# Performance work log

Hardware: AMD Instinct MI355X
Metric: run time of the kernel (lower is better)

## Reference

```python
import jax, jax.numpy as jnp
import numpy as np

# Eigenvalue spec: (alpha, omega, multiplicity); field='complex' => d_state = sum(mul)
EIGS = [(-0.4, 0.0, 32), (-0.3, 3.14, 32), (-0.2, 6.28, 32), (-0.1, 12.57, 32),
        (-0.05, 25.13, 32), (-0.02, 50.27, 32), (-0.01, 100.53, 32), (-0.005, 201.06, 32)]
DELTA_MIN, DELTA_MAX = 1e-3, 1e-1
B_SZ, H, L = 8, 128, 8192  # batch, d_input, seq length


def setup_inputs() -> dict:
    key = jax.random.key(0)
    k_delta, k_bre, k_bim, k_cre, k_cim, k_d, k_u = jax.random.split(key, 7)
    # continuous-time diagonal state matrix Lambda (P,) complex
    Lam = np.concatenate([np.full(m, a + 1j * w, dtype=np.complex64) for a, w, m in EIGS])
    Lambda = jnp.asarray(Lam)  # (P,)
    P = Lambda.shape[0]
    # ZOH discretization (done at init in the torch module)
    Delta = DELTA_MIN + (DELTA_MAX - DELTA_MIN) * jax.random.uniform(k_delta, (P,), dtype=jnp.float32)
    Lambda_bar = jnp.exp(Lambda * Delta)  # (P,) complex64
    B = (jax.random.normal(k_bre, (P, H), dtype=jnp.float32)
         + 1j * jax.random.normal(k_bim, (P, H), dtype=jnp.float32))
    B_bar = (((Lambda_bar - 1.0) / Lambda)[:, None] * B).astype(jnp.complex64)  # (P,H)
    C_re = jax.random.normal(k_cre, (H, P), dtype=jnp.float32)
    C_im = jax.random.normal(k_cim, (H, P), dtype=jnp.float32)
    D = jax.random.normal(k_d, (H, H), dtype=jnp.float32)
    u = jax.random.normal(k_u, (B_SZ, H, L), dtype=jnp.float32)
    return {
        "u": u,
        "Lambda_bar_re": jnp.real(Lambda_bar), "Lambda_bar_im": jnp.imag(Lambda_bar),
        "B_bar_re": jnp.real(B_bar), "B_bar_im": jnp.imag(B_bar),
        "C_re": C_re, "C_im": C_im, "D": D,
    }


def reference(u, Lambda_bar_re, Lambda_bar_im, B_bar_re, B_bar_im, C_re, C_im, D):
    Lambda_bar = Lambda_bar_re + 1j * Lambda_bar_im          # (P,)
    B_bar = B_bar_re + 1j * B_bar_im                         # (P,H)
    C = C_re + 1j * C_im                                     # (H,P)
    uc = u.astype(B_bar.dtype)
    Bu = jnp.einsum('ph,bhl->bpl', B_bar, uc)                # (B,P,L) complex
    A = jnp.broadcast_to(Lambda_bar[None, :, None], Bu.shape)  # (B,P,L)
    # The repo's binary op computes the sequential recurrence x_t = A_t * (x_{t-1} + Bu_t).
    # Rewriting with Bu'_t = A_t * Bu_t gives x_t = A_t x_{t-1} + Bu'_t, which is the
    # standard (truly associative) first-order scan.
    ABu = A * Bu

    def binop(ei, ej):
        a_i, b_i = ei
        a_j, b_j = ej
        return a_j * a_i, a_j * b_i + b_j

    _, xs = jax.lax.associative_scan(binop, (A, ABu), axis=2)  # xs: (B,P,L)
    y = jnp.einsum('op,bpl->bol', C, xs).real + jnp.einsum('oh,bhl->bol', D, u)
    return jax.nn.gelu(y, approximate=False)  # torch nn.GELU default = exact erf
```

## Files before the change

kernel.cpp:

```cpp
#include <hip/hip_runtime.h>
#include <math.h>

#define Bn 8
#define Hd 128
#define Ld 8192
#define Pd 256
#define LC 32
#define NC 256

typedef __attribute__((ext_vector_type(8))) short bf16x8;
typedef __attribute__((ext_vector_type(4))) float f32x4;
#define MFMA16(a, b, c) __builtin_amdgcn_mfma_f32_16x16x32_bf16(a, b, c, 0, 0, 0)

__device__ __forceinline__ unsigned short f2bf(float f) {
  unsigned u = __float_as_uint(f);
  u = u + 0x7fffu + ((u >> 16) & 1u);
  return (unsigned short)(u >> 16);
}

#if __has_builtin(__builtin_amdgcn_cvt_pk_bf16_f32)
typedef __attribute__((ext_vector_type(2))) __bf16 v2bf_t;
__device__ __forceinline__ unsigned pack2(float a, float b) {
  v2bf_t r = __builtin_amdgcn_cvt_pk_bf16_f32(a, b);
  unsigned u;
  __builtin_memcpy(&u, &r, 4);
  return u;
}
#else
__device__ __forceinline__ unsigned pack2(float a, float b) {
  return (unsigned)f2bf(a) | ((unsigned)f2bf(b) << 16);
}
#endif

__device__ __forceinline__ float bflo(unsigned v) { return __uint_as_float(v << 16); }
__device__ __forceinline__ float bfhi(unsigned v) { return __uint_as_float(v & 0xffff0000u); }

__device__ __forceinline__ int bperm(int p) {
  return ((p & 4) << 2) | ((p & 16) >> 1) | ((p & 8) >> 1) | (p & 3);
}

__global__ void k_prep(const float* __restrict__ Bre, const float* __restrict__ Bim,
                       const float* __restrict__ Cre, const float* __restrict__ Cim,
                       const float* __restrict__ Dm,
                       bf16x8* __restrict__ Bfr, bf16x8* __restrict__ Bfi,
                       bf16x8* __restrict__ Cf, bf16x8* __restrict__ Df) {
  int tid = blockIdx.x * 256 + threadIdx.x;
  int lane = tid & 63, slot = tid >> 6;
  int q = lane >> 4, ln = lane & 15;
  if (slot < 64) {
    int ks = slot >> 4, mt = slot & 15;
    int p = mt * 16 + ln;
    bf16x8 vr, vi;
#pragma unroll
    for (int e = 0; e < 8; ++e) {
      int h = ks * 32 + q * 8 + e;
      vr[e] = (short)f2bf(Bre[p * Hd + h]);
      vi[e] = (short)f2bf(Bim[p * Hd + h]);
    }
    Bfr[slot * 64 + lane] = vr;
    Bfi[slot * 64 + lane] = vi;
  } else if (slot < 64 + 128) {
    int s2 = slot - 64;
    int ks = s2 >> 3, mt = s2 & 7;
    int o = mt * 16 + ln;
    bf16x8 v;
#pragma unroll
    for (int e = 0; e < 8; ++e) {
      int kp = ks * 32 + q * 8 + e;
      int p = kp >> 1;
      float val = (kp & 1) ? -Cim[o * Pd + p] : Cre[o * Pd + p];
      v[e] = (short)f2bf(val);
    }
    Cf[s2 * 64 + lane] = v;
  } else if (slot < 64 + 128 + 32) {
    int s3 = slot - 192;
    int ks = s3 >> 3, mt = s3 & 7;
    int o = mt * 16 + ln;
    bf16x8 v;
#pragma unroll
    for (int e = 0; e < 8; ++e) {
      int h = ks * 32 + q * 8 + e;
      v[e] = (short)f2bf(Dm[o * Hd + h]);
    }
    Df[s3 * 64 + lane] = v;
  }
}

__device__ __forceinline__ void stage_u(const float* __restrict__ ub, unsigned* us32, int t) {
  int lane = t & 63, w = t >> 6;
  int j0 = 4 * (lane & 7);
  int h2 = 16 * w + 2 * (lane >> 3);
  const float* r0 = ub + (size_t)h2 * Ld + j0;
  float4 a0 = *(const float4*)r0;
  float4 a1 = *(const float4*)(r0 + Ld);
  const float* r2 = r0 + (size_t)64 * Ld;
  float4 b0 = *(const float4*)r2;
  float4 b1 = *(const float4*)(r2 + Ld);
  float ta0[4] = {a0.x, a0.y, a0.z, a0.w};
  float ta1[4] = {a1.x, a1.y, a1.z, a1.w};
  float tb0[4] = {b0.x, b0.y, b0.z, b0.w};
  float tb1[4] = {b1.x, b1.y, b1.z, b1.w};
#pragma unroll
  for (int i = 0; i < 4; ++i) {
    int j = j0 + i;
    int g1 = (h2 >> 3) ^ (j & 7);
    us32[(j * 256 + (g1 << 4) + ((2 * h2) & 15)) >> 2] = pack2(ta0[i], ta1[i]);
    int hb = h2 + 64;
    int g2 = (hb >> 3) ^ (j & 7);
    us32[(j * 256 + (g2 << 4) + ((2 * hb) & 15)) >> 2] = pack2(tb0[i], tb1[i]);
  }
}

__device__ __forceinline__ void compute_bu(const unsigned* us32,
                                           const bf16x8* __restrict__ Bfr,
                                           const bf16x8* __restrict__ Bfi,
                                           unsigned* bu32, int t) {
  int lane = t & 63, w = t >> 6, q = lane >> 4, ln = lane & 15;
  f32x4 zz = {0.f, 0.f, 0.f, 0.f};
  f32x4 aR[4][2], aI[4][2];
#pragma unroll
  for (int mt = 0; mt < 4; ++mt)
#pragma unroll
    for (int n = 0; n < 2; ++n) { aR[mt][n] = zz; aI[mt][n] = zz; }

#pragma unroll
  for (int ks = 0; ks < 4; ++ks) {
    bf16x8 ubf[2];
#pragma unroll
    for (int n = 0; n < 2; ++n) {
      int j = 16 * n + ln;
      int g = (4 * ks + q) ^ (j & 7);
      ubf[n] = *(const bf16x8*)((const char*)us32 + j * 256 + g * 16);
    }
#pragma unroll
    for (int mt = 0; mt < 4; ++mt) {
      int tI = ks * 16 + w * 4 + mt;
      bf16x8 ar = Bfr[tI * 64 + lane];
      bf16x8 ai = Bfi[tI * 64 + lane];
#pragma unroll
      for (int n = 0; n < 2; ++n) {
        aR[mt][n] = MFMA16(ar, ubf[n], aR[mt][n]);
        aI[mt][n] = MFMA16(ai, ubf[n], aI[mt][n]);
      }
    }
  }
#pragma unroll
  for (int mt = 0; mt < 4; ++mt)
#pragma unroll
    for (int n = 0; n < 2; ++n)
#pragma unroll
      for (int r = 0; r < 4; ++r) {
        int p = w * 64 + mt * 16 + q * 4 + r;
        int j = 16 * n + ln;
        bu32[(p << 5) | (j ^ bperm(p))] = pack2(aR[mt][n][r], aI[mt][n][r]);
      }
}

__global__ __launch_bounds__(256, 4) void k_chunk(
    const float* __restrict__ u, const float* __restrict__ lre,
    const float* __restrict__ lim, const bf16x8* __restrict__ Bfr,
    const bf16x8* __restrict__ Bfi, float2* __restrict__ E) {
  int bc = blockIdx.x;
  int b = bc >> 8, c = bc & 255;
  __shared__ __align__(16) unsigned char smem[8192 + 32768];
  unsigned* us32 = (unsigned*)smem;
  unsigned* bu32 = (unsigned*)(smem + 8192);
  int t = threadIdx.x;

  stage_u(u + (size_t)b * Hd * Ld + c * LC, us32, t);
  __syncthreads();
  compute_bu(us32, Bfr, Bfi, bu32, t);
  __syncthreads();

  int p = t;
  int pm = bperm(p);
  float ax = lre[p], ay = lim[p];
  float xr = 0.f, xi = 0.f;
#pragma unroll
  for (int j = 0; j < LC; ++j) {
    unsigned v = bu32[(p << 5) | (j ^ pm)];
    float sr = xr + bflo(v), si = xi + bfhi(v);
    xr = ax * sr - ay * si;
    xi = ax * si + ay * sr;
  }
  E[(size_t)bc * Pd + p] = make_float2(xr, xi);
}

__global__ __launch_bounds__(256) void k_scan(const float* __restrict__ lre,
                                              const float* __restrict__ lim,
                                              float2* __restrict__ E) {
  __shared__ float2 arr[32][8];
  int nb = blockIdx.x;
  int t = threadIdx.x;
  int pl = t & 7, rq = t >> 3;
  int b = nb >> 5;
  int p = ((nb & 31) << 3) + pl;
  float ax = lre[p], ay = lim[p];
  float mx = ax, my = ay;
#pragma unroll
  for (int k = 0; k < 5; ++k) {
    float nx = mx * mx - my * my, ny = 2.f * mx * my;
    mx = nx; my = ny;
  }
  size_t base = ((size_t)(b * NC + rq * 8)) * Pd + p;
  float2 pre[8];
  float cr = 0.f, ci = 0.f;
#pragma unroll
  for (int i = 0; i < 8; ++i) {
    float2 e = E[base + (size_t)i * Pd];
    pre[i] = make_float2(cr, ci);
    float nx = mx * cr - my * ci + e.x;
    float ny = mx * ci + my * cr + e.y;
    cr = nx; ci = ny;
  }
  float Mx = mx, My = my;
#pragma unroll
  for (int k = 0; k < 3; ++k) {
    float nx = Mx * Mx - My * My, ny = 2.f * Mx * My;
    Mx = nx; My = ny;
  }
  float Vx = cr, Vy = ci;
#pragma unroll
  for (int d = 1; d < 32; d <<= 1) {
    arr[rq][pl] = make_float2(Vx, Vy);
    __syncthreads();
    if (rq >= d) {
      float2 pv = arr[rq - d][pl];
      Vx += Mx * pv.x - My * pv.y;
      Vy += Mx * pv.y + My * pv.x;
    }
    __syncthreads();
    float nx = Mx * Mx - My * My, ny = 2.f * Mx * My;
    Mx = nx; My = ny;
  }
  arr[rq][pl] = make_float2(Vx, Vy);
  __syncthreads();
  float Cx = 0.f, Cy = 0.f;
  if (rq > 0) {
    float2 pv = arr[rq - 1][pl];
    Cx = pv.x; Cy = pv.y;
  }
  float tx = 1.f, ty = 0.f;
#pragma unroll
  for (int i = 0; i < 8; ++i) {
    float ox = pre[i].x + tx * Cx - ty * Cy;
    float oy = pre[i].y + tx * Cy + ty * Cx;
    E[base + (size_t)i * Pd] = make_float2(ox, oy);
    float nx = tx * mx - ty * my, ny = tx * my + ty * mx;
    tx = nx; ty = ny;
  }
}

__global__ __launch_bounds__(256, 4) void k_main(
    const float* __restrict__ u, const float* __restrict__ lre,
    const float* __restrict__ lim, const bf16x8* __restrict__ Bfr,
    const bf16x8* __restrict__ Bfi, const bf16x8* __restrict__ Cf,
    const bf16x8* __restrict__ Df, const float2* __restrict__ E,
    float* __restrict__ out) {
  int bc = blockIdx.x;
  int b = bc >> 8, c = bc & 255;
  __shared__ __align__(16) unsigned char smem[8192 + 32768];
  unsigned* us32 = (unsigned*)smem;
  unsigned* bu32 = (unsigned*)(smem + 8192);
  unsigned* xs32 = bu32;
  int t = threadIdx.x;
  int lane = t & 63, w = t >> 6, q = lane >> 4, ln = lane & 15;

  stage_u(u + (size_t)b * Hd * Ld + c * LC, us32, t);
  __syncthreads();
  compute_bu(us32, Bfr, Bfi, bu32, t);
  __syncthreads();

  int p = t;
  int pm = bperm(p);
  unsigned v[LC];
#pragma unroll
  for (int j = 0; j < LC; ++j) v[j] = bu32[(p << 5) | (j ^ pm)];
  float2 xin = E[(size_t)bc * Pd + p];
  __syncthreads();

  {
    float ax = lre[p], ay = lim[p];
    float xr = xin.x, xi = xin.y;
#pragma unroll
    for (int j = 0; j < LC; ++j) {
      float sr = xr + bflo(v[j]), si = xi + bfhi(v[j]);
      xr = ax * sr - ay * si;
      xi = ax * si + ay * sr;
      xs32[j * 256 + ((((p >> 2) ^ (j & 7)) << 2) + (p & 3))] = pack2(xr, xi);
    }
  }
  __syncthreads();

  f32x4 zz = {0.f, 0.f, 0.f, 0.f};
  f32x4 acc[2][2] = {{zz, zz}, {zz, zz}};
#pragma unroll
  for (int ks = 0; ks < 16; ++ks) {
    bf16x8 xb[2];
#pragma unroll
    for (int n = 0; n < 2; ++n) {
      int j = 16 * n + ln;
      int g = (4 * ks + q) ^ (j & 7);
      xb[n] = *(const bf16x8*)((const char*)xs32 + j * 1024 + g * 16);
    }
#pragma unroll
    for (int mt = 0; mt < 2; ++mt) {
      bf16x8 cf = Cf[(ks * 8 + w * 2 + mt) * 64 + lane];
#pragma unroll
      for (int n = 0; n < 2; ++n) acc[mt][n] = MFMA16(cf, xb[n], acc[mt][n]);
    }
  }
#pragma unroll
  for (int ks = 0; ks < 4; ++ks) {
    bf16x8 ubf[2];
#pragma unroll
    for (int n = 0; n < 2; ++n) {
      int j = 16 * n + ln;
      int g = (4 * ks + q) ^ (j & 7);
      ubf[n] = *(const bf16x8*)((const char*)us32 + j * 256 + g * 16);
    }
#pragma unroll
    for (int mt = 0; mt < 2; ++mt) {
      bf16x8 df = Df[(ks * 8 + w * 2 + mt) * 64 + lane];
#pragma unroll
      for (int n = 0; n < 2; ++n) acc[mt][n] = MFMA16(df, ubf[n], acc[mt][n]);
    }
  }

#pragma unroll
  for (int mt = 0; mt < 2; ++mt)
#pragma unroll
    for (int n = 0; n < 2; ++n)
#pragma unroll
      for (int r = 0; r < 4; ++r) {
        int o = w * 32 + mt * 16 + q * 4 + r;
        int l = c * LC + 16 * n + ln;
        float vy = acc[mt][n][r];
        float e2 = __builtin_amdgcn_exp2f(-2.4554670f * vy);
        float gy = vy * __builtin_amdgcn_rcpf(1.0f + e2);
        out[((size_t)(b * Hd + o)) * Ld + l] = gy;
      }
}

extern "C" void kernel_launch(void* const* d_in, const int* in_sizes, int n_in,
                              void* d_out, int out_size, void* d_ws, size_t ws_size,
                              hipStream_t stream) {
  const float* u   = (const float*)d_in[0];
  const float* lre = (const float*)d_in[1];
  const float* lim = (const float*)d_in[2];
  const float* Bre = (const float*)d_in[3];
  const float* Bim = (const float*)d_in[4];
  const float* Cre = (const float*)d_in[5];
  const float* Cim = (const float*)d_in[6];
  const float* Dm  = (const float*)d_in[7];
  float* out = (float*)d_out;

  char* ws = (char*)d_ws;
  bf16x8* Bfr = (bf16x8*)(ws);
  bf16x8* Bfi = (bf16x8*)(ws + 65536);
  bf16x8* Cf  = (bf16x8*)(ws + 131072);
  bf16x8* Df  = (bf16x8*)(ws + 262144);
  float2* E   = (float2*)(ws + (1 << 20));

  k_prep<<<56, 256, 0, stream>>>(Bre, Bim, Cre, Cim, Dm, Bfr, Bfi, Cf, Df);
  k_chunk<<<Bn * NC, 256, 0, stream>>>(u, lre, lim, Bfr, Bfi, E);
  k_scan<<<256, 256, 0, stream>>>(lre, lim, E);
  k_main<<<Bn * NC, 256, 0, stream>>>(u, lre, lim, Bfr, Bfi, Cf, Df, E, out);
}
```

Measured before the change: 147.5 us.

## Fuse chunk, scan and projection into one cooperative persistent kernel

Replaces the three-kernel chunk/scan/main sequence with one cooperative kernel of 1024 blocks that each handle two chunks. Grid-wide syncs separate the chunk-state, cross-chunk scan and projection phases. The Bu values are kept in registers between phases so the B projection and recurrence inputs are not recomputed in the final phase, and launch gaps are removed. The cost is two grid barriers, higher register pressure from holding 64 packed values per thread, and only 256 of 1024 blocks working during the scan phase; the old three-kernel path remains as a fallback if the cooperative launch is not available.

```diff
diff --git a/kernel.cpp b/kernel.cpp
--- a/kernel.cpp
+++ b/kernel.cpp
@@ -1,5 +1,8 @@
 #include <hip/hip_runtime.h>
+#include <hip/hip_cooperative_groups.h>
 #include <math.h>
+
+namespace cg = cooperative_groups;
 
 #define Bn 8
 #define Hd 128
@@ -156,6 +159,247 @@
       }
 }
 
+__device__ __forceinline__ void compute_bu_half(const unsigned* us32,
+                                                const bf16x8* __restrict__ Bfr,
+                                                const bf16x8* __restrict__ Bfi,
+                                                unsigned* bu32, int t, int mh) {
+  int lane = t & 63, w = t >> 6, q = lane >> 4, ln = lane & 15;
+  f32x4 zz = {0.f, 0.f, 0.f, 0.f};
+  f32x4 aR[2][2], aI[2][2];
+#pragma unroll
+  for (int mt = 0; mt < 2; ++mt)
+#pragma unroll
+    for (int n = 0; n < 2; ++n) { aR[mt][n] = zz; aI[mt][n] = zz; }
+
+#pragma unroll
+  for (int ks = 0; ks < 4; ++ks) {
+    bf16x8 ubf[2];
+#pragma unroll
+    for (int n = 0; n < 2; ++n) {
+      int j = 16 * n + ln;
+      int g = (4 * ks + q) ^ (j & 7);
+      ubf[n] = *(const bf16x8*)((const char*)us32 + j * 256 + g * 16);
+    }
+#pragma unroll
+    for (int mt = 0; mt < 2; ++mt) {
+      int tI = ks * 16 + w * 4 + mh * 2 + mt;
+      bf16x8 ar = Bfr[tI * 64 + lane];
+      bf16x8 ai = Bfi[tI * 64 + lane];
+#pragma unroll
+      for (int n = 0; n < 2; ++n) {
+        aR[mt][n] = MFMA16(ar, ubf[n], aR[mt][n]);
+        aI[mt][n] = MFMA16(ai, ubf[n], aI[mt][n]);
+      }
+    }
+  }
+#pragma unroll
+  for (int mt = 0; mt < 2; ++mt)
+#pragma unroll
+    for (int n = 0; n < 2; ++n)
+#pragma unroll
+      for (int r = 0; r < 4; ++r) {
+        int p = w * 64 + (mh * 2 + mt) * 16 + q * 4 + r;
+        int j = 16 * n + ln;
+        bu32[(p << 5) | (j ^ bperm(p))] = pack2(aR[mt][n][r], aI[mt][n][r]);
+      }
+}
+
+__device__ __forceinline__ void scan_rows(const float* __restrict__ lre,
+                                          const float* __restrict__ lim,
+                                          float2* __restrict__ E, int nb, int t,
+                                          float2* arr) {
+  int pl = t & 7, rq = t >> 3;
+  int b = nb >> 5;
+  int p = ((nb & 31) << 3) + pl;
+  float mx = lre[p], my = lim[p];
+#pragma unroll
+  for (int k = 0; k < 5; ++k) {
+    float nx = mx * mx - my * my, ny = 2.f * mx * my;
+    mx = nx; my = ny;
+  }
+  size_t base = ((size_t)(b * NC + rq * 8)) * Pd + p;
+  float2 pre[8];
+  float cr = 0.f, ci = 0.f;
+#pragma unroll
+  for (int i = 0; i < 8; ++i) {
+    float2 e = E[base + (size_t)i * Pd];
+    pre[i] = make_float2(cr, ci);
+    float nx = mx * cr - my * ci + e.x;
+    float ny = mx * ci + my * cr + e.y;
+    cr = nx; ci = ny;
+  }
+  float Mx = mx, My = my;
+#pragma unroll
+  for (int k = 0; k < 3; ++k) {
+    float nx = Mx * Mx - My * My, ny = 2.f * Mx * My;
+    Mx = nx; My = ny;
+  }
+  float Vx = cr, Vy = ci;
+#pragma unroll
+  for (int d = 1; d < 32; d <<= 1) {
+    arr[rq * 8 + pl] = make_float2(Vx, Vy);
+    __syncthreads();
+    if (rq >= d) {
+      float2 pv = arr[(rq - d) * 8 + pl];
+      Vx += Mx * pv.x - My * pv.y;
+      Vy += Mx * pv.y + My * pv.x;
+    }
+    __syncthreads();
+    float nx = Mx * Mx - My * My, ny = 2.f * Mx * My;
+    Mx = nx; My = ny;
+  }
+  arr[rq * 8 + pl] = make_float2(Vx, Vy);
+  __syncthreads();
+  float Cx = 0.f, Cy = 0.f;
+  if (rq > 0) {
+    float2 pv = arr[(rq - 1) * 8 + pl];
+    Cx = pv.x; Cy = pv.y;
+  }
+  float tx = 1.f, ty = 0.f;
+#pragma unroll
+  for (int i = 0; i < 8; ++i) {
+    float ox = pre[i].x + tx * Cx - ty * Cy;
+    float oy = pre[i].y + tx * Cy + ty * Cx;
+    E[base + (size_t)i * Pd] = make_float2(ox, oy);
+    float nx = tx * mx - ty * my, ny = tx * my + ty * mx;
+    tx = nx; ty = ny;
+  }
+}
+
+__device__ __forceinline__ void project_one(const bf16x8* __restrict__ Cf,
+                                            const bf16x8* __restrict__ Df,
+                                            const unsigned* us32, const unsigned* xs32,
+                                            float* __restrict__ out, int b, int c, int t) {
+  int lane = t & 63, w = t >> 6, q = lane >> 4, ln = lane & 15;
+  f32x4 zz = {0.f, 0.f, 0.f, 0.f};
+  f32x4 acc[2][2] = {{zz, zz}, {zz, zz}};
+#pragma unroll
+  for (int ks = 0; ks < 16; ++ks) {
+    bf16x8 xb[2];
+#pragma unroll
+    for (int n = 0; n < 2; ++n) {
+      int j = 16 * n + ln;
+      int g = (4 * ks + q) ^ (j & 7);
+      xb[n] = *(const bf16x8*)((const char*)xs32 + j * 1024 + g * 16);
+    }
+#pragma unroll
+    for (int mt = 0; mt < 2; ++mt) {
+      bf16x8 cf = Cf[(ks * 8 + w * 2 + mt) * 64 + lane];
+#pragma unroll
+      for (int n = 0; n < 2; ++n) acc[mt][n] = MFMA16(cf, xb[n], acc[mt][n]);
+    }
+  }
+#pragma unroll
+  for (int ks = 0; ks < 4; ++ks) {
+    bf16x8 ubf[2];
+#pragma unroll
+    for (int n = 0; n < 2; ++n) {
+      int j = 16 * n + ln;
+      int g = (4 * ks + q) ^ (j & 7);
+      ubf[n] = *(const bf16x8*)((const char*)us32 + j * 256 + g * 16);
+    }
+#pragma unroll
+    for (int mt = 0; mt < 2; ++mt) {
+      bf16x8 df = Df[(ks * 8 + w * 2 + mt) * 64 + lane];
+#pragma unroll
+      for (int n = 0; n < 2; ++n) acc[mt][n] = MFMA16(df, ubf[n], acc[mt][n]);
+    }
+  }
+#pragma unroll
+  for (int mt = 0; mt < 2; ++mt)
+#pragma unroll
+    for (int n = 0; n < 2; ++n)
+#pragma unroll
+      for (int r = 0; r < 4; ++r) {
+        int o = w * 32 + mt * 16 + q * 4 + r;
+        int l = c * LC + 16 * n + ln;
+        float vy = acc[mt][n][r];
+        float e2 = __builtin_amdgcn_exp2f(-2.4554670f * vy);
+        float gy = vy * __builtin_amdgcn_rcpf(1.0f + e2);
+        out[((size_t)(b * Hd + o)) * Ld + l] = gy;
+      }
+}
+
+__device__ __forceinline__ void phaseA_one(const float* __restrict__ u,
+                                           const bf16x8* __restrict__ Bfr,
+                                           const bf16x8* __restrict__ Bfi,
+                                           float2* __restrict__ E, unsigned* us32,
+                                           unsigned* bu32, int t, int bc, float ax,
+                                           float ay, int pm, unsigned (&vv)[LC]) {
+  int b = bc >> 8, c = bc & 255;
+  int p = t;
+  stage_u(u + (size_t)b * Hd * Ld + c * LC, us32, t);
+  __syncthreads();
+  compute_bu_half(us32, Bfr, Bfi, bu32, t, 0);
+  compute_bu_half(us32, Bfr, Bfi, bu32, t, 1);
+  __syncthreads();
+  float xr = 0.f, xi = 0.f;
+#pragma unroll
+  for (int j = 0; j < LC; ++j) {
+    unsigned w = bu32[(p << 5) | (j ^ pm)];
+    vv[j] = w;
+    float sr = xr + bflo(w), si = xi + bfhi(w);
+    xr = ax * sr - ay * si;
+    xi = ax * si + ay * sr;
+  }
+  E[(size_t)bc * Pd + p] = make_float2(xr, xi);
+}
+
+template <bool RESTAGE>
+__device__ __forceinline__ void phaseC_one(const float* __restrict__ u,
+                                           const bf16x8* __restrict__ Cf,
+                                           const bf16x8* __restrict__ Df,
+                                           const float2* __restrict__ E,
+                                           float* __restrict__ out, unsigned* us32,
+                                           unsigned* xs32, int t, int bc, float ax,
+                                           float ay, const unsigned (&vv)[LC]) {
+  int b = bc >> 8, c = bc & 255;
+  int p = t;
+  if (RESTAGE) stage_u(u + (size_t)b * Hd * Ld + c * LC, us32, t);
+  float2 xin = E[(size_t)bc * Pd + p];
+  float xr = xin.x, xi = xin.y;
+#pragma unroll
+  for (int j = 0; j < LC; ++j) {
+    unsigned w = vv[j];
+    float sr = xr + bflo(w), si = xi + bfhi(w);
+    xr = ax * sr - ay * si;
+    xi = ax * si + ay * sr;
+    xs32[j * 256 + ((((p >> 2) ^ (j & 7)) << 2) + (p & 3))] = pack2(xr, xi);
+  }
+  __syncthreads();
+  project_one(Cf, Df, us32, xs32, out, b, c, t);
+}
+
+__global__ __launch_bounds__(256, 4) void k_fused(
+    const float* __restrict__ u, const float* __restrict__ lre,
+    const float* __restrict__ lim, const bf16x8* __restrict__ Bfr,
+    const bf16x8* __restrict__ Bfi, const bf16x8* __restrict__ Cf,
+    const bf16x8* __restrict__ Df, float2* __restrict__ E,
+    float* __restrict__ out) {
+  cg::grid_group grid = cg::this_grid();
+  int blk = blockIdx.x;
+  __shared__ __align__(16) unsigned char smem[8192 + 32768];
+  unsigned* us32 = (unsigned*)smem;
+  unsigned* bu32 = (unsigned*)(smem + 8192);
+  int t = threadIdx.x;
+  int p = t, pm = bperm(p);
+  float ax = lre[p], ay = lim[p];
+  unsigned v0[LC], v1[LC];
+
+  phaseA_one(u, Bfr, Bfi, E, us32, bu32, t, 2 * blk + 0, ax, ay, pm, v0);
+  phaseA_one(u, Bfr, Bfi, E, us32, bu32, t, 2 * blk + 1, ax, ay, pm, v1);
+  __threadfence();
+  grid.sync();
+
+  if (blk < 256) scan_rows(lre, lim, E, blk, t, (float2*)bu32);
+  __threadfence();
+  grid.sync();
+
+  phaseC_one<false>(u, Cf, Df, E, out, us32, bu32, t, 2 * blk + 1, ax, ay, v1);
+  __syncthreads();
+  phaseC_one<true>(u, Cf, Df, E, out, us32, bu32, t, 2 * blk + 0, ax, ay, v0);
+}
+
 __global__ __launch_bounds__(256, 4) void k_chunk(
     const float* __restrict__ u, const float* __restrict__ lre,
     const float* __restrict__ lim, const bf16x8* __restrict__ Bfr,
@@ -189,66 +433,8 @@
 __global__ __launch_bounds__(256) void k_scan(const float* __restrict__ lre,
                                               const float* __restrict__ lim,
                                               float2* __restrict__ E) {
-  __shared__ float2 arr[32][8];
-  int nb = blockIdx.x;
-  int t = threadIdx.x;
-  int pl = t & 7, rq = t >> 3;
-  int b = nb >> 5;
-  int p = ((nb & 31) << 3) + pl;
-  float ax = lre[p], ay = lim[p];
-  float mx = ax, my = ay;
-#pragma unroll
-  for (int k = 0; k < 5; ++k) {
-    float nx = mx * mx - my * my, ny = 2.f * mx * my;
-    mx = nx; my = ny;
-  }
-  size_t base = ((size_t)(b * NC + rq * 8)) * Pd + p;
-  float2 pre[8];
-  float cr = 0.f, ci = 0.f;
-#pragma unroll
-  for (int i = 0; i < 8; ++i) {
-    float2 e = E[base + (size_t)i * Pd];
-    pre[i] = make_float2(cr, ci);
-    float nx = mx * cr - my * ci + e.x;
-    float ny = mx * ci + my * cr + e.y;
-    cr = nx; ci = ny;
-  }
-  float Mx = mx, My = my;
-#pragma unroll
-  for (int k = 0; k < 3; ++k) {
-    float nx = Mx * Mx - My * My, ny = 2.f * Mx * My;
-    Mx = nx; My = ny;
-  }
-  float Vx = cr, Vy = ci;
-#pragma unroll
-  for (int d = 1; d < 32; d <<= 1) {
-    arr[rq][pl] = make_float2(Vx, Vy);
-    __syncthreads();
-    if (rq >= d) {
-      float2 pv = arr[rq - d][pl];
-      Vx += Mx * pv.x - My * pv.y;
-      Vy += Mx * pv.y + My * pv.x;
-    }
-    __syncthreads();
-    float nx = Mx * Mx - My * My, ny = 2.f * Mx * My;
-    Mx = nx; My = ny;
-  }
-  arr[rq][pl] = make_float2(Vx, Vy);
-  __syncthreads();
-  float Cx = 0.f, Cy = 0.f;
-  if (rq > 0) {
-    float2 pv = arr[rq - 1][pl];
-    Cx = pv.x; Cy = pv.y;
-  }
-  float tx = 1.f, ty = 0.f;
-#pragma unroll
-  for (int i = 0; i < 8; ++i) {
-    float ox = pre[i].x + tx * Cx - ty * Cy;
-    float oy = pre[i].y + tx * Cy + ty * Cx;
-    E[base + (size_t)i * Pd] = make_float2(ox, oy);
-    float nx = tx * mx - ty * my, ny = tx * my + ty * mx;
-    tx = nx; ty = ny;
-  }
+  __shared__ float2 arr[32 * 8];
+  scan_rows(lre, lim, E, blockIdx.x, threadIdx.x, arr);
 }
 
 __global__ __launch_bounds__(256, 4) void k_main(
@@ -264,7 +450,6 @@
   unsigned* bu32 = (unsigned*)(smem + 8192);
   unsigned* xs32 = bu32;
   int t = threadIdx.x;
-  int lane = t & 63, w = t >> 6, q = lane >> 4, ln = lane & 15;
 
   stage_u(u + (size_t)b * Hd * Ld + c * LC, us32, t);
   __syncthreads();
@@ -291,55 +476,7 @@
     }
   }
   __syncthreads();
-
-  f32x4 zz = {0.f, 0.f, 0.f, 0.f};
-  f32x4 acc[2][2] = {{zz, zz}, {zz, zz}};
-#pragma unroll
-  for (int ks = 0; ks < 16; ++ks) {
-    bf16x8 xb[2];
-#pragma unroll
-    for (int n = 0; n < 2; ++n) {
-      int j = 16 * n + ln;
-      int g = (4 * ks + q) ^ (j & 7);
-      xb[n] = *(const bf16x8*)((const char*)xs32 + j * 1024 + g * 16);
-    }
-#pragma unroll
-    for (int mt = 0; mt < 2; ++mt) {
-      bf16x8 cf = Cf[(ks * 8 + w * 2 + mt) * 64 + lane];
-#pragma unroll
-      for (int n = 0; n < 2; ++n) acc[mt][n] = MFMA16(cf, xb[n], acc[mt][n]);
-    }
-  }
-#pragma unroll
-  for (int ks = 0; ks < 4; ++ks) {
-    bf16x8 ubf[2];
-#pragma unroll
-    for (int n = 0; n < 2; ++n) {
-      int j = 16 * n + ln;
-      int g = (4 * ks + q) ^ (j & 7);
-      ubf[n] = *(const bf16x8*)((const char*)us32 + j * 256 + g * 16);
-    }
-#pragma unroll
-    for (int mt = 0; mt < 2; ++mt) {
-      bf16x8 df = Df[(ks * 8 + w * 2 + mt) * 64 + lane];
-#pragma unroll
-      for (int n = 0; n < 2; ++n) acc[mt][n] = MFMA16(df, ubf[n], acc[mt][n]);
-    }
-  }
-
-#pragma unroll
-  for (int mt = 0; mt < 2; ++mt)
-#pragma unroll
-    for (int n = 0; n < 2; ++n)
-#pragma unroll
-      for (int r = 0; r < 4; ++r) {
-        int o = w * 32 + mt * 16 + q * 4 + r;
-        int l = c * LC + 16 * n + ln;
-        float vy = acc[mt][n][r];
-        float e2 = __builtin_amdgcn_exp2f(-2.4554670f * vy);
-        float gy = vy * __builtin_amdgcn_rcpf(1.0f + e2);
-        out[((size_t)(b * Hd + o)) * Ld + l] = gy;
-      }
+  project_one(Cf, Df, us32, xs32, out, b, c, t);
 }
 
 extern "C" void kernel_launch(void* const* d_in, const int* in_sizes, int n_in,
@@ -362,7 +499,25 @@
   bf16x8* Df  = (bf16x8*)(ws + 262144);
   float2* E   = (float2*)(ws + (1 << 20));
 
+  static int coop = -1;
+  if (coop < 0) {
+    int nb = 0;
+    hipError_t oe = hipOccupancyMaxActiveBlocksPerMultiprocessor(&nb, k_fused, 256, 0);
+    coop = (oe == hipSuccess && nb >= 4) ? 1 : 0;
+  }
+
   k_prep<<<56, 256, 0, stream>>>(Bre, Bim, Cre, Cim, Dm, Bfr, Bfi, Cf, Df);
+
+  if (coop == 1) {
+    void* kargs[] = {(void*)&u,   (void*)&lre, (void*)&lim, (void*)&Bfr,
+                     (void*)&Bfi, (void*)&Cf,  (void*)&Df,  (void*)&E,
+                     (void*)&out};
+    hipError_t err = hipLaunchCooperativeKernel((void*)k_fused, dim3(1024),
+                                                dim3(256), kargs, 0, stream);
+    if (err == hipSuccess) return;
+    coop = 0;
+  }
+
   k_chunk<<<Bn * NC, 256, 0, stream>>>(u, lre, lim, Bfr, Bfi, E);
   k_scan<<<256, 256, 0, stream>>>(lre, lim, E);
   k_main<<<Bn * NC, 256, 0, stream>>>(u, lre, lim, Bfr, Bfi, Cf, Df, E, out);
```

Result: no change. 148.4 us (+0.6%).

## Compute zero-state chunk output in first pass, add carried-state correction later

Applied to the files above, without the earlier changes.

The first chunk kernel now computes the zero-initial-state scan output C·x0 + D·u and writes it to a workspace buffer. The final kernel then only adds the contribution of the incoming carry, which is a geometric series in Lambda_bar times the carry, so it no longer restages u or recomputes B·u. This removes the duplicate Bu GEMM and u load from the second pass. In exchange it adds a full-size fp32 intermediate write and read, of the same size as the output, plus extra MFMA work in the first pass.

```diff
diff --git a/kernel.cpp b/kernel.cpp
--- a/kernel.cpp
+++ b/kernel.cpp
@@ -156,16 +156,20 @@
       }
 }
 
-__global__ __launch_bounds__(256, 4) void k_chunk(
+__global__ __launch_bounds__(256, 4) void k_chunkP(
     const float* __restrict__ u, const float* __restrict__ lre,
     const float* __restrict__ lim, const bf16x8* __restrict__ Bfr,
-    const bf16x8* __restrict__ Bfi, float2* __restrict__ E) {
+    const bf16x8* __restrict__ Bfi, const bf16x8* __restrict__ Cf,
+    const bf16x8* __restrict__ Df, float2* __restrict__ E,
+    float* __restrict__ p0out) {
   int bc = blockIdx.x;
   int b = bc >> 8, c = bc & 255;
   __shared__ __align__(16) unsigned char smem[8192 + 32768];
   unsigned* us32 = (unsigned*)smem;
   unsigned* bu32 = (unsigned*)(smem + 8192);
+  unsigned* xs32 = bu32;
   int t = threadIdx.x;
+  int lane = t & 63, w = t >> 6, q = lane >> 4, ln = lane & 15;
 
   stage_u(u + (size_t)b * Hd * Ld + c * LC, us32, t);
   __syncthreads();
@@ -174,16 +178,68 @@
 
   int p = t;
   int pm = bperm(p);
-  float ax = lre[p], ay = lim[p];
-  float xr = 0.f, xi = 0.f;
-#pragma unroll
-  for (int j = 0; j < LC; ++j) {
-    unsigned v = bu32[(p << 5) | (j ^ pm)];
-    float sr = xr + bflo(v), si = xi + bfhi(v);
-    xr = ax * sr - ay * si;
-    xi = ax * si + ay * sr;
-  }
-  E[(size_t)bc * Pd + p] = make_float2(xr, xi);
+  unsigned v[LC];
+#pragma unroll
+  for (int j = 0; j < LC; ++j) v[j] = bu32[(p << 5) | (j ^ pm)];
+  __syncthreads();
+
+  {
+    float ax = lre[p], ay = lim[p];
+    float xr = 0.f, xi = 0.f;
+#pragma unroll
+    for (int j = 0; j < LC; ++j) {
+      float sr = xr + bflo(v[j]), si = xi + bfhi(v[j]);
+      xr = ax * sr - ay * si;
+      xi = ax * si + ay * sr;
+      xs32[j * 256 + ((((p >> 2) ^ (j & 7)) << 2) + (p & 3))] = pack2(xr, xi);
+    }
+    E[(size_t)bc * Pd + p] = make_float2(xr, xi);
+  }
+  __syncthreads();
+
+  f32x4 zz = {0.f, 0.f, 0.f, 0.f};
+  f32x4 acc[2][2] = {{zz, zz}, {zz, zz}};
+#pragma unroll
+  for (int ks = 0; ks < 16; ++ks) {
+    bf16x8 xb[2];
+#pragma unroll
+    for (int n = 0; n < 2; ++n) {
+      int j = 16 * n + ln;
+      int g = (4 * ks + q) ^ (j & 7);
+      xb[n] = *(const bf16x8*)((const char*)xs32 + j * 1024 + g * 16);
+    }
+#pragma unroll
+    for (int mt = 0; mt < 2; ++mt) {
+      bf16x8 cf = Cf[(ks * 8 + w * 2 + mt) * 64 + lane];
+#pragma unroll
+      for (int n = 0; n < 2; ++n) acc[mt][n] = MFMA16(cf, xb[n], acc[mt][n]);
+    }
+  }
+#pragma unroll
+  for (int ks = 0; ks < 4; ++ks) {
+    bf16x8 ubf[2];
+#pragma unroll
+    for (int n = 0; n < 2; ++n) {
+      int j = 16 * n + ln;
+      int g = (4 * ks + q) ^ (j & 7);
+      ubf[n] = *(const bf16x8*)((const char*)us32 + j * 256 + g * 16);
+    }
+#pragma unroll
+    for (int mt = 0; mt < 2; ++mt) {
+      bf16x8 df = Df[(ks * 8 + w * 2 + mt) * 64 + lane];
+#pragma unroll
+      for (int n = 0; n < 2; ++n) acc[mt][n] = MFMA16(df, ubf[n], acc[mt][n]);
+    }
+  }
+#pragma unroll
+  for (int mt = 0; mt < 2; ++mt)
+#pragma unroll
+    for (int n = 0; n < 2; ++n)
+#pragma unroll
+      for (int r = 0; r < 4; ++r) {
+        int o = w * 32 + mt * 16 + q * 4 + r;
+        p0out[((size_t)bc * Hd + o) * LC + 16 * n + ln] = acc[mt][n][r];
+      }
 }
 
 __global__ __launch_bounds__(256) void k_scan(const float* __restrict__ lre,
@@ -251,44 +307,37 @@
   }
 }
 
-__global__ __launch_bounds__(256, 4) void k_main(
-    const float* __restrict__ u, const float* __restrict__ lre,
-    const float* __restrict__ lim, const bf16x8* __restrict__ Bfr,
-    const bf16x8* __restrict__ Bfi, const bf16x8* __restrict__ Cf,
-    const bf16x8* __restrict__ Df, const float2* __restrict__ E,
-    float* __restrict__ out) {
+__global__ __launch_bounds__(256, 4) void k_main2(
+    const float* __restrict__ lre, const float* __restrict__ lim,
+    const bf16x8* __restrict__ Cf, const float2* __restrict__ E,
+    const float* __restrict__ p0in, float* __restrict__ out) {
   int bc = blockIdx.x;
   int b = bc >> 8, c = bc & 255;
-  __shared__ __align__(16) unsigned char smem[8192 + 32768];
-  unsigned* us32 = (unsigned*)smem;
-  unsigned* bu32 = (unsigned*)(smem + 8192);
-  unsigned* xs32 = bu32;
+  __shared__ __align__(16) unsigned xs32[LC * 256];
   int t = threadIdx.x;
   int lane = t & 63, w = t >> 6, q = lane >> 4, ln = lane & 15;
 
-  stage_u(u + (size_t)b * Hd * Ld + c * LC, us32, t);
-  __syncthreads();
-  compute_bu(us32, Bfr, Bfi, bu32, t);
-  __syncthreads();
+  float p0[16];
+#pragma unroll
+  for (int mt = 0; mt < 2; ++mt)
+#pragma unroll
+    for (int n = 0; n < 2; ++n)
+#pragma unroll
+      for (int r = 0; r < 4; ++r) {
+        int o = w * 32 + mt * 16 + q * 4 + r;
+        p0[mt * 8 + n * 4 + r] = p0in[((size_t)bc * Hd + o) * LC + 16 * n + ln];
+      }
 
   int p = t;
-  int pm = bperm(p);
-  unsigned v[LC];
-#pragma unroll
-  for (int j = 0; j < LC; ++j) v[j] = bu32[(p << 5) | (j ^ pm)];
   float2 xin = E[(size_t)bc * Pd + p];
-  __syncthreads();
-
-  {
-    float ax = lre[p], ay = lim[p];
-    float xr = xin.x, xi = xin.y;
-#pragma unroll
-    for (int j = 0; j < LC; ++j) {
-      float sr = xr + bflo(v[j]), si = xi + bfhi(v[j]);
-      xr = ax * sr - ay * si;
-      xi = ax * si + ay * sr;
-      xs32[j * 256 + ((((p >> 2) ^ (j & 7)) << 2) + (p & 3))] = pack2(xr, xi);
-    }
+  float ax = lre[p], ay = lim[p];
+  float gr = ax * xin.x - ay * xin.y;
+  float gi = ax * xin.y + ay * xin.x;
+#pragma unroll
+  for (int j = 0; j < LC; ++j) {
+    xs32[j * 256 + ((((p >> 2) ^ (j & 7)) << 2) + (p & 3))] = pack2(gr, gi);
+    float nr = ax * gr - ay * gi, ni = ax * gi + ay * gr;
+    gr = nr; gi = ni;
   }
   __syncthreads();
 
@@ -310,22 +359,6 @@
       for (int n = 0; n < 2; ++n) acc[mt][n] = MFMA16(cf, xb[n], acc[mt][n]);
     }
   }
-#pragma unroll
-  for (int ks = 0; ks < 4; ++ks) {
-    bf16x8 ubf[2];
-#pragma unroll
-    for (int n = 0; n < 2; ++n) {
-      int j = 16 * n + ln;
-      int g = (4 * ks + q) ^ (j & 7);
-      ubf[n] = *(const bf16x8*)((const char*)us32 + j * 256 + g * 16);
-    }
-#pragma unroll
-    for (int mt = 0; mt < 2; ++mt) {
-      bf16x8 df = Df[(ks * 8 + w * 2 + mt) * 64 + lane];
-#pragma unroll
-      for (int n = 0; n < 2; ++n) acc[mt][n] = MFMA16(df, ubf[n], acc[mt][n]);
-    }
-  }
 
 #pragma unroll
   for (int mt = 0; mt < 2; ++mt)
@@ -335,7 +368,7 @@
       for (int r = 0; r < 4; ++r) {
         int o = w * 32 + mt * 16 + q * 4 + r;
         int l = c * LC + 16 * n + ln;
-        float vy = acc[mt][n][r];
+        float vy = acc[mt][n][r] + p0[mt * 8 + n * 4 + r];
         float e2 = __builtin_amdgcn_exp2f(-2.4554670f * vy);
         float gy = vy * __builtin_amdgcn_rcpf(1.0f + e2);
         out[((size_t)(b * Hd + o)) * Ld + l] = gy;
@@ -360,10 +393,11 @@
   bf16x8* Bfi = (bf16x8*)(ws + 65536);
   bf16x8* Cf  = (bf16x8*)(ws + 131072);
   bf16x8* Df  = (bf16x8*)(ws + 262144);
-  float2* E   = (float2*)(ws + (1 << 20));
+  float2* E   = (float2*)(ws + (1u << 20));
+  float*  P0  = (float*)(ws + (16u << 20));
 
   k_prep<<<56, 256, 0, stream>>>(Bre, Bim, Cre, Cim, Dm, Bfr, Bfi, Cf, Df);
-  k_chunk<<<Bn * NC, 256, 0, stream>>>(u, lre, lim, Bfr, Bfi, E);
+  k_chunkP<<<Bn * NC, 256, 0, stream>>>(u, lre, lim, Bfr, Bfi, Cf, Df, E, P0);
   k_scan<<<256, 256, 0, stream>>>(lre, lim, E);
-  k_main<<<Bn * NC, 256, 0, stream>>>(u, lre, lim, Bfr, Bfi, Cf, Df, E, out);
-}
+  k_main2<<<Bn * NC, 256, 0, stream>>>(lre, lim, Cf, E, P0, out);
+}
```

New measurement: 148.4 us. About the same (+0.6%).

## Write Bu directly in xs layout and scan in place without barriers

Applied to the files above, without the earlier changes.

compute_bu now stores its MFMA results straight into the swizzled xs layout with 128-bit stores, replacing the separate bperm-permuted bu buffer and its scalar stores. Both kernels then scan in place over that buffer, so k_main no longer needs the 32-entry register array or the extra copy into xs. Two __syncthreads are dropped. This relies on each wave writing exactly the p rows that it later reads. The E and Lambda loads are hoisted ahead of the u staging to overlap their latency.

```diff
diff --git a/kernel.cpp b/kernel.cpp
--- a/kernel.cpp
+++ b/kernel.cpp
@@ -35,8 +35,8 @@
 __device__ __forceinline__ float bflo(unsigned v) { return __uint_as_float(v << 16); }
 __device__ __forceinline__ float bfhi(unsigned v) { return __uint_as_float(v & 0xffff0000u); }
 
-__device__ __forceinline__ int bperm(int p) {
-  return ((p & 4) << 2) | ((p & 16) >> 1) | ((p & 8) >> 1) | (p & 3);
+__device__ __forceinline__ int xs_idx(int p, int j) {
+  return j * 256 + ((((p >> 2) ^ (j & 7)) << 2) | (p & 3));
 }
 
 __global__ void k_prep(const float* __restrict__ Bre, const float* __restrict__ Bim,
@@ -114,7 +114,7 @@
 __device__ __forceinline__ void compute_bu(const unsigned* us32,
                                            const bf16x8* __restrict__ Bfr,
                                            const bf16x8* __restrict__ Bfi,
-                                           unsigned* bu32, int t) {
+                                           unsigned* xs32, int t) {
   int lane = t & 63, w = t >> 6, q = lane >> 4, ln = lane & 15;
   f32x4 zz = {0.f, 0.f, 0.f, 0.f};
   f32x4 aR[4][2], aI[4][2];
@@ -147,13 +147,16 @@
 #pragma unroll
   for (int mt = 0; mt < 4; ++mt)
 #pragma unroll
-    for (int n = 0; n < 2; ++n)
-#pragma unroll
-      for (int r = 0; r < 4; ++r) {
-        int p = w * 64 + mt * 16 + q * 4 + r;
-        int j = 16 * n + ln;
-        bu32[(p << 5) | (j ^ bperm(p))] = pack2(aR[mt][n][r], aI[mt][n][r]);
-      }
+    for (int n = 0; n < 2; ++n) {
+      int p0 = w * 64 + mt * 16 + q * 4;
+      int j = 16 * n + ln;
+      int g = (p0 >> 2) ^ (j & 7);
+      uint4 wv = make_uint4(pack2(aR[mt][n][0], aI[mt][n][0]),
+                            pack2(aR[mt][n][1], aI[mt][n][1]),
+                            pack2(aR[mt][n][2], aI[mt][n][2]),
+                            pack2(aR[mt][n][3], aI[mt][n][3]));
+      *(uint4*)(xs32 + j * 256 + g * 4) = wv;
+    }
 }
 
 __global__ __launch_bounds__(256, 4) void k_chunk(
@@ -164,21 +167,19 @@
   int b = bc >> 8, c = bc & 255;
   __shared__ __align__(16) unsigned char smem[8192 + 32768];
   unsigned* us32 = (unsigned*)smem;
-  unsigned* bu32 = (unsigned*)(smem + 8192);
+  unsigned* xs32 = (unsigned*)(smem + 8192);
   int t = threadIdx.x;
 
   stage_u(u + (size_t)b * Hd * Ld + c * LC, us32, t);
   __syncthreads();
-  compute_bu(us32, Bfr, Bfi, bu32, t);
-  __syncthreads();
+  compute_bu(us32, Bfr, Bfi, xs32, t);
 
   int p = t;
-  int pm = bperm(p);
   float ax = lre[p], ay = lim[p];
   float xr = 0.f, xi = 0.f;
 #pragma unroll
   for (int j = 0; j < LC; ++j) {
-    unsigned v = bu32[(p << 5) | (j ^ pm)];
+    unsigned v = xs32[xs_idx(p, j)];
     float sr = xr + bflo(v), si = xi + bfhi(v);
     xr = ax * sr - ay * si;
     xi = ax * si + ay * sr;
@@ -261,33 +262,28 @@
   int b = bc >> 8, c = bc & 255;
   __shared__ __align__(16) unsigned char smem[8192 + 32768];
   unsigned* us32 = (unsigned*)smem;
-  unsigned* bu32 = (unsigned*)(smem + 8192);
-  unsigned* xs32 = bu32;
+  unsigned* xs32 = (unsigned*)(smem + 8192);
   int t = threadIdx.x;
   int lane = t & 63, w = t >> 6, q = lane >> 4, ln = lane & 15;
+  int p = t;
+
+  float2 xin = E[(size_t)bc * Pd + p];
+  float ax = lre[p], ay = lim[p];
 
   stage_u(u + (size_t)b * Hd * Ld + c * LC, us32, t);
   __syncthreads();
-  compute_bu(us32, Bfr, Bfi, bu32, t);
-  __syncthreads();
-
-  int p = t;
-  int pm = bperm(p);
-  unsigned v[LC];
-#pragma unroll
-  for (int j = 0; j < LC; ++j) v[j] = bu32[(p << 5) | (j ^ pm)];
-  float2 xin = E[(size_t)bc * Pd + p];
-  __syncthreads();
+  compute_bu(us32, Bfr, Bfi, xs32, t);
 
   {
-    float ax = lre[p], ay = lim[p];
     float xr = xin.x, xi = xin.y;
 #pragma unroll
     for (int j = 0; j < LC; ++j) {
-      float sr = xr + bflo(v[j]), si = xi + bfhi(v[j]);
+      int idx = xs_idx(p, j);
+      unsigned v = xs32[idx];
+      float sr = xr + bflo(v), si = xi + bfhi(v);
       xr = ax * sr - ay * si;
       xi = ax * si + ay * sr;
-      xs32[j * 256 + ((((p >> 2) ^ (j & 7)) << 2) + (p & 3))] = pack2(xr, xi);
+      xs32[idx] = pack2(xr, xi);
     }
   }
   __syncthreads();
```

Result: no change. 145.3 us (-1.5%).
